# Optimization experiments

Hardware: AMD Instinct MI355X
Metric: run time of the kernel (lower is better)

## Reference

```python
import jax, jax.numpy as jnp
import numpy as np


def grid_sample_bilinear(feat, grid):
    """Bilinear grid_sample, align_corners=False, zeros padding.
    feat: [B, C, H, W]; grid: [B, N, 2] with (x, y) in [-1, 1]. Returns [B, C, N].
    """
    B, C, H, W = feat.shape
    gx, gy = grid[..., 0], grid[..., 1]
    # unnormalize (align_corners=False): pixel = ((g + 1) * size - 1) / 2
    ix = ((gx + 1.0) * W - 1.0) * 0.5
    iy = ((gy + 1.0) * H - 1.0) * 0.5
    x0 = jnp.floor(ix)
    y0 = jnp.floor(iy)
    x1 = x0 + 1.0
    y1 = y0 + 1.0
    wx1 = ix - x0
    wx0 = 1.0 - wx1
    wy1 = iy - y0
    wy0 = 1.0 - wy1
    featf = feat.reshape(B, C, H * W)

    def corner(xi, yi, w):
        valid = (xi >= 0) & (xi <= W - 1) & (yi >= 0) & (yi <= H - 1)
        xi_c = jnp.clip(xi, 0, W - 1).astype(jnp.int32)
        yi_c = jnp.clip(yi, 0, H - 1).astype(jnp.int32)
        idx = yi_c * W + xi_c                                  # [B, N]
        vals = jnp.take_along_axis(featf, idx[:, None, :], axis=2)  # [B, C, N]
        return vals * (w * valid.astype(feat.dtype))[:, None, :]

    return (corner(x0, y0, wx0 * wy0) + corner(x1, y0, wx1 * wy0)
            + corner(x0, y1, wx0 * wy1) + corner(x1, y1, wx1 * wy1))


def setup_inputs() -> dict:
    key = jax.random.key(0)
    ks = jax.random.split(key, 8)
    B_T, C, H, W = 128, 256, 64, 64
    J = 17
    n_heads, n_points = 8, 4
    HP = n_heads * n_points
    video_features = jax.random.normal(ks[0], (B_T, C, H, W), dtype=jnp.float32)
    reference_points = jax.random.uniform(ks[1], (B_T, J, 2), dtype=jnp.float32,
                                          minval=-1.0, maxval=1.0)
    # offset predictor: Linear(C -> HP*2); weights init small like the module
    W_off = 0.01 * jax.random.normal(ks[2], (C, HP * 2), dtype=jnp.float32)
    b_off = 0.01 * jax.random.normal(ks[3], (HP * 2,), dtype=jnp.float32)
    # weight predictor: Linear(C -> HP)
    W_w = 0.01 * jax.random.normal(ks[4], (C, HP), dtype=jnp.float32)
    b_w = jnp.zeros((HP,), dtype=jnp.float32)
    # output projection: Linear(C -> C), xavier-ish scale
    W_out = jax.random.normal(ks[5], (C, C), dtype=jnp.float32) * (1.0 / np.sqrt(C))
    b_out = jnp.zeros((C,), dtype=jnp.float32)
    return {"video_features": video_features, "reference_points": reference_points,
            "W_off": W_off, "b_off": b_off, "W_w": W_w, "b_w": b_w,
            "W_out": W_out, "b_out": b_out}


def reference(video_features, reference_points, W_off, b_off, W_w, b_w, W_out, b_out):
    B, C, H, W = video_features.shape
    J = reference_points.shape[1]
    HP = W_w.shape[1]  # n_heads * n_points
    # initial queries: sample features at reference points -> [B, J, C]
    q = grid_sample_bilinear(video_features, reference_points).transpose(0, 2, 1)
    # learned fractional offsets: [B, J, HP, 2]
    offsets = (q @ W_off + b_off).reshape(B, J, HP, 2)
    # softmax attention weights over all heads*points: [B, J, HP]
    weights = jax.nn.softmax(q @ W_w + b_w, axis=-1)
    # final sampling grid, clamped to valid range: [B, J*HP, 2]
    grid = jnp.clip(reference_points[:, :, None, :] + offsets, -1.0, 1.0)
    grid = grid.reshape(B, J * HP, 2)
    # sample and weighted-sum: [B, C, J, HP] x [B, J, HP] -> [B, J, C]
    sampled = grid_sample_bilinear(video_features, grid).reshape(B, C, J, HP)
    out = jnp.einsum('bcjp,bjp->bjc', sampled, weights)
    return out @ W_out + b_out
```

## Files before the change

### kernel.cpp

```cpp
#include <hip/hip_runtime.h>

#define B_  128
#define C_  256
#define H_  64
#define W_  64
#define J_  17
#define HP_ 32
#define HW_ (H_ * W_)
#define CG_ 2

__global__ __launch_bounds__(256)
void pass12_kernel(const float* __restrict__ feat,
                   const float* __restrict__ refpts,
                   const float* __restrict__ Woff,
                   const float* __restrict__ boff,
                   const float* __restrict__ Ww,
                   const float* __restrict__ bw,
                   int4*  __restrict__ meta_idx,
                   float4* __restrict__ meta_w)
{
    __shared__ float q_lds[C_];
    __shared__ float part_off[4][64];
    __shared__ float part_w[8][32];
    __shared__ float off_lds[2 * HP_];
    __shared__ float logit_lds[HP_];

    const int bj = blockIdx.x;
    const int b  = bj / J_;
    const int j  = bj % J_;
    const int c  = threadIdx.x;

    const float rx = refpts[(b * J_ + j) * 2 + 0];
    const float ry = refpts[(b * J_ + j) * 2 + 1];

    {
        const float* featbc = feat + (size_t)(b * C_ + c) * HW_;
        float ix = (rx + 1.0f) * (0.5f * W_) - 0.5f;
        float iy = (ry + 1.0f) * (0.5f * H_) - 0.5f;
        float x0f = floorf(ix), y0f = floorf(iy);
        int x0 = (int)x0f, y0 = (int)y0f;
        int x1 = x0 + 1,  y1 = y0 + 1;
        float wx1 = ix - x0f, wx0 = 1.0f - wx1;
        float wy1 = iy - y0f, wy0 = 1.0f - wy1;
        bool vx0 = (x0 >= 0) && (x0 < W_);
        bool vx1 = (x1 >= 0) && (x1 < W_);
        bool vy0 = (y0 >= 0) && (y0 < H_);
        bool vy1 = (y1 >= 0) && (y1 < H_);
        int x0c = min(max(x0, 0), W_ - 1), x1c = min(max(x1, 0), W_ - 1);
        int y0c = min(max(y0, 0), H_ - 1), y1c = min(max(y1, 0), H_ - 1);
        float v00 = (vx0 && vy0) ? featbc[y0c * W_ + x0c] : 0.0f;
        float v10 = (vx1 && vy0) ? featbc[y0c * W_ + x1c] : 0.0f;
        float v01 = (vx0 && vy1) ? featbc[y1c * W_ + x0c] : 0.0f;
        float v11 = (vx1 && vy1) ? featbc[y1c * W_ + x1c] : 0.0f;
        q_lds[c] = v00 * (wx0 * wy0) + v10 * (wx1 * wy0)
                 + v01 * (wx0 * wy1) + v11 * (wx1 * wy1);
    }
    __syncthreads();

    {
        const int wv = c >> 6, ln = c & 63;
        float aoff = 0.0f;
        #pragma unroll 8
        for (int i = 0; i < 64; ++i) {
            const int k = wv * 64 + i;
            aoff += q_lds[k] * Woff[k * 64 + ln];
        }
        part_off[wv][ln] = aoff;
        const int h = ln >> 5, p = ln & 31;
        float aw = 0.0f;
        #pragma unroll 8
        for (int i = 0; i < 32; ++i) {
            const int k = wv * 64 + h * 32 + i;
            aw += q_lds[k] * Ww[k * 32 + p];
        }
        part_w[wv * 2 + h][p] = aw;
    }
    __syncthreads();
    if (c < 64) {
        off_lds[c] = boff[c] + part_off[0][c] + part_off[1][c]
                   + part_off[2][c] + part_off[3][c];
    } else if (c < 96) {
        const int p = c - 64;
        float s = bw[p];
        #pragma unroll
        for (int sidx = 0; sidx < 8; ++sidx) s += part_w[sidx][p];
        logit_lds[p] = s;
    }
    __syncthreads();

    if (c < HP_) {
        float l = logit_lds[c];
        float m = l;
        #pragma unroll
        for (int mask = 16; mask >= 1; mask >>= 1) m = fmaxf(m, __shfl_xor(m, mask));
        float e = expf(l - m);
        float s = e;
        #pragma unroll
        for (int mask = 16; mask >= 1; mask >>= 1) s += __shfl_xor(s, mask);
        const float ww = e / s;

        float gx = fminf(fmaxf(rx + off_lds[2 * c + 0], -1.0f), 1.0f);
        float gy = fminf(fmaxf(ry + off_lds[2 * c + 1], -1.0f), 1.0f);
        float ix = (gx + 1.0f) * (0.5f * W_) - 0.5f;
        float iy = (gy + 1.0f) * (0.5f * H_) - 0.5f;
        float x0f = floorf(ix), y0f = floorf(iy);
        int x0 = (int)x0f, y0 = (int)y0f;
        int x1 = x0 + 1,  y1 = y0 + 1;
        float wx1 = ix - x0f, wx0 = 1.0f - wx1;
        float wy1 = iy - y0f, wy0 = 1.0f - wy1;
        float v00 = (float)((x0 >= 0) && (x0 < W_) && (y0 >= 0) && (y0 < H_));
        float v10 = (float)((x1 >= 0) && (x1 < W_) && (y0 >= 0) && (y0 < H_));
        float v01 = (float)((x0 >= 0) && (x0 < W_) && (y1 >= 0) && (y1 < H_));
        float v11 = (float)((x1 >= 0) && (x1 < W_) && (y1 >= 0) && (y1 < H_));
        int x0c = min(max(x0, 0), W_ - 1), x1c = min(max(x1, 0), W_ - 1);
        int y0c = min(max(y0, 0), H_ - 1), y1c = min(max(y1, 0), H_ - 1);
        const int mi = bj * HP_ + c;
        meta_idx[mi] = make_int4(y0c * W_ + x0c, y0c * W_ + x1c,
                                 y1c * W_ + x0c, y1c * W_ + x1c);
        meta_w[mi] = make_float4(ww * wx0 * wy0 * v00, ww * wx1 * wy0 * v10,
                                 ww * wx0 * wy1 * v01, ww * wx1 * wy1 * v11);
    }
}

__global__ __launch_bounds__(256)
void gather_kernel(const float* __restrict__ feat,
                   const int4*  __restrict__ meta_idx,
                   const float4* __restrict__ meta_w,
                   float* __restrict__ acc)
{
    __shared__ float plane[CG_ * HW_];

    const int blk = blockIdx.x;
    const int b   = blk >> 7;
    const int cg  = blk & 127;
    const int c0  = cg * CG_;
    const int t   = threadIdx.x;
    const int wv  = t >> 6;
    const int ln  = t & 63;

    {
        const char* gsrc = (const char*)(feat + (size_t)(b * C_ + c0) * HW_);
        #pragma unroll
        for (int i = 0; i < 8; ++i) {
            const size_t off = ((size_t)(i * 256 + wv * 64)) * 16;
            __builtin_amdgcn_global_load_lds(
                (const __attribute__((address_space(1))) void*)(gsrc + off + (size_t)ln * 16),
                (__attribute__((address_space(3))) void*)((char*)plane + off),
                16, 0, 0);
        }
    }

    const int p    = ln & 31;
    const int half = ln >> 5;
    int4   id_r[3];
    float4 w_r[3];
    #pragma unroll
    for (int iter = 0; iter < 3; ++iter) {
        const int j = iter * 8 + wv * 2 + half;
        if (j < J_) {
            const int mi = (b * J_ + j) * HP_ + p;
            id_r[iter] = meta_idx[mi];
            w_r[iter]  = meta_w[mi];
        } else {
            id_r[iter] = make_int4(0, 0, 0, 0);
            w_r[iter]  = make_float4(0.f, 0.f, 0.f, 0.f);
        }
    }
    __syncthreads();

    #pragma unroll
    for (int iter = 0; iter < 3; ++iter) {
        const int j = iter * 8 + wv * 2 + half;
        const int4   id = id_r[iter];
        const float4 w  = w_r[iter];
        float pj0 = w.x * plane[id.x] + w.y * plane[id.y]
                  + w.z * plane[id.z] + w.w * plane[id.w];
        float pj1 = w.x * plane[HW_ + id.x] + w.y * plane[HW_ + id.y]
                  + w.z * plane[HW_ + id.z] + w.w * plane[HW_ + id.w];
        #pragma unroll
        for (int mask = 16; mask >= 1; mask >>= 1) {
            pj0 += __shfl_xor(pj0, mask);
            pj1 += __shfl_xor(pj1, mask);
        }
        if (j < J_ && p == 0) {
            float2* dst = (float2*)(acc + ((size_t)(b * J_ + j)) * C_ + c0);
            *dst = make_float2(pj0, pj1);
        }
    }
}

#define PROJ_ROWS 8
__global__ __launch_bounds__(256)
void proj_kernel(const float* __restrict__ acc,
                 const float* __restrict__ Wout,
                 const float* __restrict__ bout,
                 float* __restrict__ out)
{
    __shared__ float a_lds[PROJ_ROWS][C_];
    const int bj0 = blockIdx.x * PROJ_ROWS;
    const int t   = threadIdx.x;

    #pragma unroll
    for (int r = 0; r < PROJ_ROWS; ++r)
        a_lds[r][t] = acc[(size_t)(bj0 + r) * C_ + t];
    __syncthreads();

    const int c = t;
    float o[PROJ_ROWS];
    const float bb = bout[c];
    #pragma unroll
    for (int r = 0; r < PROJ_ROWS; ++r) o[r] = bb;

    #pragma unroll 4
    for (int k = 0; k < C_; ++k) {
        const float wv = Wout[(size_t)k * C_ + c];
        #pragma unroll
        for (int r = 0; r < PROJ_ROWS; ++r)
            o[r] += a_lds[r][k] * wv;
    }

    #pragma unroll
    for (int r = 0; r < PROJ_ROWS; ++r)
        out[(size_t)(bj0 + r) * C_ + c] = o[r];
}

__device__ __forceinline__ float bilin_sample(const float* __restrict__ featc,
                                              float gx, float gy) {
    float ix = (gx + 1.0f) * (0.5f * W_) - 0.5f;
    float iy = (gy + 1.0f) * (0.5f * H_) - 0.5f;
    float x0f = floorf(ix), y0f = floorf(iy);
    int x0 = (int)x0f, y0 = (int)y0f;
    int x1 = x0 + 1,  y1 = y0 + 1;
    float wx1 = ix - x0f, wx0 = 1.0f - wx1;
    float wy1 = iy - y0f, wy0 = 1.0f - wy1;
    bool vx0 = (x0 >= 0) && (x0 < W_);
    bool vx1 = (x1 >= 0) && (x1 < W_);
    bool vy0 = (y0 >= 0) && (y0 < H_);
    bool vy1 = (y1 >= 0) && (y1 < H_);
    int x0c = min(max(x0, 0), W_ - 1), x1c = min(max(x1, 0), W_ - 1);
    int y0c = min(max(y0, 0), H_ - 1), y1c = min(max(y1, 0), H_ - 1);
    float v00 = (vx0 && vy0) ? featc[y0c * W_ + x0c] : 0.0f;
    float v10 = (vx1 && vy0) ? featc[y0c * W_ + x1c] : 0.0f;
    float v01 = (vx0 && vy1) ? featc[y1c * W_ + x0c] : 0.0f;
    float v11 = (vx1 && vy1) ? featc[y1c * W_ + x1c] : 0.0f;
    return v00 * (wx0 * wy0) + v10 * (wx1 * wy0)
         + v01 * (wx0 * wy1) + v11 * (wx1 * wy1);
}

__global__ __launch_bounds__(256)
void msdks_kernel(const float* __restrict__ feat,
                  const float* __restrict__ refpts,
                  const float* __restrict__ Woff,
                  const float* __restrict__ boff,
                  const float* __restrict__ Ww,
                  const float* __restrict__ bw,
                  const float* __restrict__ Wout,
                  const float* __restrict__ bout,
                  float* __restrict__ out)
{
    __shared__ float q_lds[C_];
    __shared__ float off_lds[2 * HP_];
    __shared__ float logit_lds[HP_];
    __shared__ float wgt_lds[HP_];
    __shared__ float gx_lds[HP_];
    __shared__ float gy_lds[HP_];
    __shared__ float acc_lds[C_];

    const int bj = blockIdx.x;
    const int b  = bj / J_;
    const int j  = bj % J_;
    const int c  = threadIdx.x;

    const float rx = refpts[(b * J_ + j) * 2 + 0];
    const float ry = refpts[(b * J_ + j) * 2 + 1];
    const float* featbc = feat + (size_t)(b * C_ + c) * HW_;

    q_lds[c] = bilin_sample(featbc, rx, ry);
    __syncthreads();

    if (c < 64) {
        float s = boff[c];
        for (int k = 0; k < C_; ++k) s += q_lds[k] * Woff[k * 64 + c];
        off_lds[c] = s;
    } else if (c < 96) {
        const int p = c - 64;
        float s = bw[p];
        for (int k = 0; k < C_; ++k) s += q_lds[k] * Ww[k * HP_ + p];
        logit_lds[p] = s;
    }
    __syncthreads();

    if (c < HP_) {
        float l = logit_lds[c];
        float m = l;
        for (int mask = 16; mask; mask >>= 1) m = fmaxf(m, __shfl_xor(m, mask));
        float e = expf(l - m);
        float s = e;
        for (int mask = 16; mask; mask >>= 1) s += __shfl_xor(s, mask);
        wgt_lds[c] = e / s;
        gx_lds[c] = fminf(fmaxf(rx + off_lds[c * 2 + 0], -1.0f), 1.0f);
        gy_lds[c] = fminf(fmaxf(ry + off_lds[c * 2 + 1], -1.0f), 1.0f);
    }
    __syncthreads();

    float acc = 0.0f;
    for (int pp = 0; pp < HP_; ++pp)
        acc += wgt_lds[pp] * bilin_sample(featbc, gx_lds[pp], gy_lds[pp]);
    acc_lds[c] = acc;
    __syncthreads();

    float o = bout[c];
    for (int k = 0; k < C_; ++k) o += acc_lds[k] * Wout[k * C_ + c];
    out[(size_t)(b * J_ + j) * C_ + c] = o;
}

extern "C" void kernel_launch(void* const* d_in, const int* in_sizes, int n_in,
                              void* d_out, int out_size, void* d_ws, size_t ws_size,
                              hipStream_t stream) {
    const float* feat   = (const float*)d_in[0];
    const float* refpts = (const float*)d_in[1];
    const float* Woff   = (const float*)d_in[2];
    const float* boff   = (const float*)d_in[3];
    const float* Ww     = (const float*)d_in[4];
    const float* bw     = (const float*)d_in[5];
    const float* Wout   = (const float*)d_in[6];
    const float* bout   = (const float*)d_in[7];
    float* out = (float*)d_out;

    const size_t n_meta    = (size_t)B_ * J_ * HP_;
    const size_t idx_bytes = n_meta * sizeof(int4);
    const size_t w_bytes   = n_meta * sizeof(float4);
    const size_t acc_bytes = (size_t)B_ * J_ * C_ * sizeof(float);

    if (ws_size >= idx_bytes + w_bytes + acc_bytes) {
        char* ws = (char*)d_ws;
        int4*   meta_idx = (int4*)ws;
        float4* meta_w   = (float4*)(ws + idx_bytes);
        float*  acc      = (float*)(ws + idx_bytes + w_bytes);

        pass12_kernel<<<dim3(B_ * J_), dim3(256), 0, stream>>>(
            feat, refpts, Woff, boff, Ww, bw, meta_idx, meta_w);
        gather_kernel<<<dim3(B_ * (C_ / CG_)), dim3(256), 0, stream>>>(
            feat, meta_idx, meta_w, acc);
        proj_kernel<<<dim3((B_ * J_) / PROJ_ROWS), dim3(256), 0, stream>>>(
            acc, Wout, bout, out);
    } else {
        msdks_kernel<<<dim3(B_ * J_), dim3(256), 0, stream>>>(
            feat, refpts, Woff, boff, Ww, bw, Wout, bout, out);
    }
}
```

Baseline: 162.2 us.

## Make gather kernel persistent with double-buffered LDS prefetch of feature planes

The gather kernel now launches 2048 blocks, each handling 8 consecutive (batch, channel-pair) tasks. The next task's two feature planes are prefetched into a second LDS buffer via global_load_lds while the current planes are sampled, so the global-to-LDS load overlaps the bilinear gathers. The fallback fused kernel and the workspace-size check are removed. LDS per block doubles to 64KB, which reduces how many blocks fit per CU and may lower occupancy.

```diff
diff --git a/kernel.cpp b/kernel.cpp
--- a/kernel.cpp
+++ b/kernel.cpp
@@ -8,6 +8,10 @@
 #define HP_ 32
 #define HW_ (H_ * W_)
 #define CG_ 2
+#define GBLK_ 2048
+#define NTASK (B_ * (C_ / CG_))
+#define TASKS_PER_BLK (NTASK / GBLK_)
+#define PROJ_ROWS 8
 
 __global__ __launch_bounds__(256)
 void pass12_kernel(const float* __restrict__ feat,
@@ -122,74 +126,94 @@
     }
 }
 
+__device__ __forceinline__ void stage_task(const float* __restrict__ feat,
+                                           int task, float* buf, int t) {
+    const int b   = task >> 7;
+    const int cgp = task & 127;
+    const int wv  = t >> 6;
+    const int ln  = t & 63;
+    const char* gsrc = (const char*)(feat + (size_t)(b * C_ + cgp * CG_) * HW_);
+    #pragma unroll
+    for (int i = 0; i < 8; ++i) {
+        const size_t off = ((size_t)(i * 256 + wv * 64)) * 16;
+        __builtin_amdgcn_global_load_lds(
+            (const __attribute__((address_space(1))) void*)(gsrc + off + (size_t)ln * 16),
+            (__attribute__((address_space(3))) void*)((char*)buf + off),
+            16, 0, 0);
+    }
+}
+
 __global__ __launch_bounds__(256)
 void gather_kernel(const float* __restrict__ feat,
                    const int4*  __restrict__ meta_idx,
                    const float4* __restrict__ meta_w,
                    float* __restrict__ acc)
 {
-    __shared__ float plane[CG_ * HW_];
+    __shared__ float lds[2 * CG_ * HW_];
 
     const int blk = blockIdx.x;
-    const int b   = blk >> 7;
-    const int cg  = blk & 127;
-    const int c0  = cg * CG_;
     const int t   = threadIdx.x;
     const int wv  = t >> 6;
     const int ln  = t & 63;
-
-    {
-        const char* gsrc = (const char*)(feat + (size_t)(b * C_ + c0) * HW_);
-        #pragma unroll
-        for (int i = 0; i < 8; ++i) {
-            const size_t off = ((size_t)(i * 256 + wv * 64)) * 16;
-            __builtin_amdgcn_global_load_lds(
-                (const __attribute__((address_space(1))) void*)(gsrc + off + (size_t)ln * 16),
-                (__attribute__((address_space(3))) void*)((char*)plane + off),
-                16, 0, 0);
-        }
-    }
-
     const int p    = ln & 31;
     const int half = ln >> 5;
-    int4   id_r[3];
-    float4 w_r[3];
-    #pragma unroll
-    for (int iter = 0; iter < 3; ++iter) {
-        const int j = iter * 8 + wv * 2 + half;
-        if (j < J_) {
-            const int mi = (b * J_ + j) * HP_ + p;
-            id_r[iter] = meta_idx[mi];
-            w_r[iter]  = meta_w[mi];
-        } else {
-            id_r[iter] = make_int4(0, 0, 0, 0);
-            w_r[iter]  = make_float4(0.f, 0.f, 0.f, 0.f);
-        }
-    }
-    __syncthreads();
-
-    #pragma unroll
-    for (int iter = 0; iter < 3; ++iter) {
-        const int j = iter * 8 + wv * 2 + half;
-        const int4   id = id_r[iter];
-        const float4 w  = w_r[iter];
-        float pj0 = w.x * plane[id.x] + w.y * plane[id.y]
-                  + w.z * plane[id.z] + w.w * plane[id.w];
-        float pj1 = w.x * plane[HW_ + id.x] + w.y * plane[HW_ + id.y]
-                  + w.z * plane[HW_ + id.z] + w.w * plane[HW_ + id.w];
-        #pragma unroll
-        for (int mask = 16; mask >= 1; mask >>= 1) {
-            pj0 += __shfl_xor(pj0, mask);
-            pj1 += __shfl_xor(pj1, mask);
-        }
-        if (j < J_ && p == 0) {
-            float2* dst = (float2*)(acc + ((size_t)(b * J_ + j)) * C_ + c0);
-            *dst = make_float2(pj0, pj1);
-        }
-    }
-}
-
-#define PROJ_ROWS 8
+
+    const int task0 = blk * TASKS_PER_BLK;
+
+    stage_task(feat, task0, lds, t);
+    __syncthreads();
+
+    #pragma unroll 1
+    for (int r = 0; r < TASKS_PER_BLK; ++r) {
+        const int task = task0 + r;
+        const int b    = task >> 7;
+        const int c0   = (task & 127) * CG_;
+        float* cur = lds + (r & 1) * (CG_ * HW_);
+
+        int4   id_r[3];
+        float4 w_r[3];
+        #pragma unroll
+        for (int iter = 0; iter < 3; ++iter) {
+            const int j = iter * 8 + wv * 2 + half;
+            if (j < J_) {
+                const int mi = (b * J_ + j) * HP_ + p;
+                id_r[iter] = meta_idx[mi];
+                w_r[iter]  = meta_w[mi];
+            } else {
+                id_r[iter] = make_int4(0, 0, 0, 0);
+                w_r[iter]  = make_float4(0.f, 0.f, 0.f, 0.f);
+            }
+        }
+        __builtin_amdgcn_sched_barrier(0);
+
+        if (r + 1 < TASKS_PER_BLK)
+            stage_task(feat, task + 1, lds + ((r + 1) & 1) * (CG_ * HW_), t);
+        __builtin_amdgcn_sched_barrier(0);
+
+        #pragma unroll
+        for (int iter = 0; iter < 3; ++iter) {
+            const int j = iter * 8 + wv * 2 + half;
+            const int4   id = id_r[iter];
+            const float4 w  = w_r[iter];
+            float pj0 = w.x * cur[id.x] + w.y * cur[id.y]
+                      + w.z * cur[id.z] + w.w * cur[id.w];
+            float pj1 = w.x * cur[HW_ + id.x] + w.y * cur[HW_ + id.y]
+                      + w.z * cur[HW_ + id.z] + w.w * cur[HW_ + id.w];
+            #pragma unroll
+            for (int mask = 16; mask >= 1; mask >>= 1) {
+                pj0 += __shfl_xor(pj0, mask);
+                pj1 += __shfl_xor(pj1, mask);
+            }
+            if (j < J_ && p == 0) {
+                float2* dst = (float2*)(acc + ((size_t)(b * J_ + j)) * C_ + c0);
+                *dst = make_float2(pj0, pj1);
+            }
+        }
+
+        __syncthreads();
+    }
+}
+
 __global__ __launch_bounds__(256)
 void proj_kernel(const float* __restrict__ acc,
                  const float* __restrict__ Wout,
@@ -205,113 +229,20 @@
         a_lds[r][t] = acc[(size_t)(bj0 + r) * C_ + t];
     __syncthreads();
 
-    const int c = t;
     float o[PROJ_ROWS];
-    const float bb = bout[c];
+    const float bb = bout[t];
     #pragma unroll
     for (int r = 0; r < PROJ_ROWS; ++r) o[r] = bb;
-
     #pragma unroll 4
     for (int k = 0; k < C_; ++k) {
-        const float wv = Wout[(size_t)k * C_ + c];
+        const float wvv = Wout[(size_t)k * C_ + t];
         #pragma unroll
         for (int r = 0; r < PROJ_ROWS; ++r)
-            o[r] += a_lds[r][k] * wv;
-    }
-
+            o[r] += a_lds[r][k] * wvv;
+    }
     #pragma unroll
     for (int r = 0; r < PROJ_ROWS; ++r)
-        out[(size_t)(bj0 + r) * C_ + c] = o[r];
-}
-
-__device__ __forceinline__ float bilin_sample(const float* __restrict__ featc,
-                                              float gx, float gy) {
-    float ix = (gx + 1.0f) * (0.5f * W_) - 0.5f;
-    float iy = (gy + 1.0f) * (0.5f * H_) - 0.5f;
-    float x0f = floorf(ix), y0f = floorf(iy);
-    int x0 = (int)x0f, y0 = (int)y0f;
-    int x1 = x0 + 1,  y1 = y0 + 1;
-    float wx1 = ix - x0f, wx0 = 1.0f - wx1;
-    float wy1 = iy - y0f, wy0 = 1.0f - wy1;
-    bool vx0 = (x0 >= 0) && (x0 < W_);
-    bool vx1 = (x1 >= 0) && (x1 < W_);
-    bool vy0 = (y0 >= 0) && (y0 < H_);
-    bool vy1 = (y1 >= 0) && (y1 < H_);
-    int x0c = min(max(x0, 0), W_ - 1), x1c = min(max(x1, 0), W_ - 1);
-    int y0c = min(max(y0, 0), H_ - 1), y1c = min(max(y1, 0), H_ - 1);
-    float v00 = (vx0 && vy0) ? featc[y0c * W_ + x0c] : 0.0f;
-    float v10 = (vx1 && vy0) ? featc[y0c * W_ + x1c] : 0.0f;
-    float v01 = (vx0 && vy1) ? featc[y1c * W_ + x0c] : 0.0f;
-    float v11 = (vx1 && vy1) ? featc[y1c * W_ + x1c] : 0.0f;
-    return v00 * (wx0 * wy0) + v10 * (wx1 * wy0)
-         + v01 * (wx0 * wy1) + v11 * (wx1 * wy1);
-}
-
-__global__ __launch_bounds__(256)
-void msdks_kernel(const float* __restrict__ feat,
-                  const float* __restrict__ refpts,
-                  const float* __restrict__ Woff,
-                  const float* __restrict__ boff,
-                  const float* __restrict__ Ww,
-                  const float* __restrict__ bw,
-                  const float* __restrict__ Wout,
-                  const float* __restrict__ bout,
-                  float* __restrict__ out)
-{
-    __shared__ float q_lds[C_];
-    __shared__ float off_lds[2 * HP_];
-    __shared__ float logit_lds[HP_];
-    __shared__ float wgt_lds[HP_];
-    __shared__ float gx_lds[HP_];
-    __shared__ float gy_lds[HP_];
-    __shared__ float acc_lds[C_];
-
-    const int bj = blockIdx.x;
-    const int b  = bj / J_;
-    const int j  = bj % J_;
-    const int c  = threadIdx.x;
-
-    const float rx = refpts[(b * J_ + j) * 2 + 0];
-    const float ry = refpts[(b * J_ + j) * 2 + 1];
-    const float* featbc = feat + (size_t)(b * C_ + c) * HW_;
-
-    q_lds[c] = bilin_sample(featbc, rx, ry);
-    __syncthreads();
-
-    if (c < 64) {
-        float s = boff[c];
-        for (int k = 0; k < C_; ++k) s += q_lds[k] * Woff[k * 64 + c];
-        off_lds[c] = s;
-    } else if (c < 96) {
-        const int p = c - 64;
-        float s = bw[p];
-        for (int k = 0; k < C_; ++k) s += q_lds[k] * Ww[k * HP_ + p];
-        logit_lds[p] = s;
-    }
-    __syncthreads();
-
-    if (c < HP_) {
-        float l = logit_lds[c];
-        float m = l;
-        for (int mask = 16; mask; mask >>= 1) m = fmaxf(m, __shfl_xor(m, mask));
-        float e = expf(l - m);
-        float s = e;
-        for (int mask = 16; mask; mask >>= 1) s += __shfl_xor(s, mask);
-        wgt_lds[c] = e / s;
-        gx_lds[c] = fminf(fmaxf(rx + off_lds[c * 2 + 0], -1.0f), 1.0f);
-        gy_lds[c] = fminf(fmaxf(ry + off_lds[c * 2 + 1], -1.0f), 1.0f);
-    }
-    __syncthreads();
-
-    float acc = 0.0f;
-    for (int pp = 0; pp < HP_; ++pp)
-        acc += wgt_lds[pp] * bilin_sample(featbc, gx_lds[pp], gy_lds[pp]);
-    acc_lds[c] = acc;
-    __syncthreads();
-
-    float o = bout[c];
-    for (int k = 0; k < C_; ++k) o += acc_lds[k] * Wout[k * C_ + c];
-    out[(size_t)(b * J_ + j) * C_ + c] = o;
+        out[(size_t)(bj0 + r) * C_ + t] = o[r];
 }
 
 extern "C" void kernel_launch(void* const* d_in, const int* in_sizes, int n_in,
@@ -330,22 +261,16 @@
     const size_t n_meta    = (size_t)B_ * J_ * HP_;
     const size_t idx_bytes = n_meta * sizeof(int4);
     const size_t w_bytes   = n_meta * sizeof(float4);
-    const size_t acc_bytes = (size_t)B_ * J_ * C_ * sizeof(float);
-
-    if (ws_size >= idx_bytes + w_bytes + acc_bytes) {
-        char* ws = (char*)d_ws;
-        int4*   meta_idx = (int4*)ws;
-        float4* meta_w   = (float4*)(ws + idx_bytes);
-        float*  acc      = (float*)(ws + idx_bytes + w_bytes);
-
-        pass12_kernel<<<dim3(B_ * J_), dim3(256), 0, stream>>>(
-            feat, refpts, Woff, boff, Ww, bw, meta_idx, meta_w);
-        gather_kernel<<<dim3(B_ * (C_ / CG_)), dim3(256), 0, stream>>>(
-            feat, meta_idx, meta_w, acc);
-        proj_kernel<<<dim3((B_ * J_) / PROJ_ROWS), dim3(256), 0, stream>>>(
-            acc, Wout, bout, out);
-    } else {
-        msdks_kernel<<<dim3(B_ * J_), dim3(256), 0, stream>>>(
-            feat, refpts, Woff, boff, Ww, bw, Wout, bout, out);
-    }
-}
+
+    char* ws = (char*)d_ws;
+    int4*   meta_idx = (int4*)ws;
+    float4* meta_w   = (float4*)(ws + idx_bytes);
+    float*  acc      = (float*)(ws + idx_bytes + w_bytes);
+
+    pass12_kernel<<<dim3(B_ * J_), dim3(256), 0, stream>>>(
+        feat, refpts, Woff, boff, Ww, bw, meta_idx, meta_w);
+    gather_kernel<<<dim3(GBLK_), dim3(256), 0, stream>>>(
+        feat, meta_idx, meta_w, acc);
+    proj_kernel<<<dim3((B_ * J_) / PROJ_ROWS), dim3(256), 0, stream>>>(
+        acc, Wout, bout, out);
+}
```

Result: slower. 180.2 us (+11.1%).
